# Performance work log

Hardware: AMD Instinct MI355X
Metric: run time of the kernel (lower is better)

Reference implementation:

```python
import jax, jax.numpy as jnp
import numpy as np

N = 100000
E = 1600000
IN_DIM = 128
OUT_DIM = 128
K = 2
LN_EPS = 1e-5


def setup_inputs() -> dict:
    key = jax.random.key(0)
    k1, k2, k3, k4 = jax.random.split(key, 4)
    x = jax.random.normal(k1, (N, IN_DIM), dtype=jnp.float32)
    edge_index = jax.random.randint(k2, (2, E), 0, N, dtype=jnp.int64)
    # LayerNorm params (elementwise affine, torch defaults)
    ln_w = jnp.ones((IN_DIM,), dtype=jnp.float32)
    ln_b = jnp.zeros((IN_DIM,), dtype=jnp.float32)
    # SGConv linear params (torch nn.Linear layout: [out, in])
    bound = 1.0 / np.sqrt(IN_DIM)
    W = jax.random.uniform(k3, (OUT_DIM, IN_DIM), minval=-bound, maxval=bound, dtype=jnp.float32)
    b = jax.random.uniform(k4, (OUT_DIM,), minval=-bound, maxval=bound, dtype=jnp.float32)
    return {"x": x, "edge_index": edge_index, "ln_w": ln_w, "ln_b": ln_b, "W": W, "b": b}


def _layer_norm(x, w, b):
    mu = jnp.mean(x, axis=-1, keepdims=True)
    var = jnp.mean(jnp.square(x - mu), axis=-1, keepdims=True)
    return (x - mu) * jax.lax.rsqrt(var + LN_EPS) * w + b


def _sgc_propagate(x, edge_index):
    # gcn_norm with added self-loops: A_hat = D^{-1/2} (A + I) D^{-1/2}
    src, dst = edge_index[0], edge_index[1]
    loop = jnp.arange(N, dtype=src.dtype)
    src_a = jnp.concatenate([src, loop])
    dst_a = jnp.concatenate([dst, loop])
    deg = jax.ops.segment_sum(jnp.ones((E + N,), dtype=x.dtype), dst_a, num_segments=N)
    dinv = jnp.where(deg > 0, jax.lax.rsqrt(jnp.maximum(deg, 1e-12)), 0.0)
    w = dinv[src_a] * dinv[dst_a]  # [E+N]
    for _ in range(K):
        x = jax.ops.segment_sum(x[src_a] * w[:, None], dst_a, num_segments=N)
    return x


def reference(x, edge_index, ln_w, ln_b, W, b):
    y = _layer_norm(x, ln_w, ln_b)
    y = _sgc_propagate(y, edge_index)
    return y @ W.T + b
```

## Files before the change

kernel.cpp:

```cpp
#include <hip/hip_runtime.h>
#include <hip/hip_fp16.h>

#define DIM 128
#define BKT_SHIFT 8
#define BKT_NODES 256
#define CHUNK 4096
#define MAXBUK 1024
#define ZROW 136

typedef _Float16 half8 __attribute__((ext_vector_type(8)));
typedef float f32x4 __attribute__((ext_vector_type(4)));


__global__ __launch_bounds__(1024) void k_s1_hist(const int* __restrict__ ei, int* __restrict__ H,
                                                  int E, int NBUK, int NBLK) {
    __shared__ int hist[MAXBUK];
    int b = blockIdx.x, tid = threadIdx.x;
    for (int i = tid; i < NBUK; i += 1024) hist[i] = 0;
    __syncthreads();
    int e0 = b * CHUNK, e1 = min(e0 + CHUNK, E);
    for (int e = e0 + tid; e < e1; e += 1024) {
        int dst = ei[E + e];
        atomicAdd(&hist[dst >> BKT_SHIFT], 1);
    }
    __syncthreads();
    for (int k = tid; k < NBUK; k += 1024) H[(size_t)k * NBLK + b] = hist[k];
}


__global__ __launch_bounds__(256) void k_scanA(const int* __restrict__ in, int* __restrict__ tmp,
                                               int* __restrict__ bsum, int n) {
    __shared__ int s[256];
    int tid = threadIdx.x;
    int i = blockIdx.x * 256 + tid;
    int v = (i < n) ? in[i] : 0;
    s[tid] = v;
    __syncthreads();
    for (int off = 1; off < 256; off <<= 1) {
        int t = (tid >= off) ? s[tid - off] : 0;
        __syncthreads();
        s[tid] += t;
        __syncthreads();
    }
    if (i < n) tmp[i] = s[tid];
    if (tid == 255) bsum[blockIdx.x] = s[255];
}

__global__ __launch_bounds__(1024) void k_scanB(int* __restrict__ bsum, int nb) {
    __shared__ int s[1024];
    int tid = threadIdx.x;
    int v = (tid < nb) ? bsum[tid] : 0;
    s[tid] = v;
    __syncthreads();
    for (int off = 1; off < 1024; off <<= 1) {
        int t = (tid >= off) ? s[tid - off] : 0;
        __syncthreads();
        s[tid] += t;
        __syncthreads();
    }
    if (tid < nb) bsum[tid] = s[tid] - v;
}

__global__ __launch_bounds__(256) void k_scanE(int* __restrict__ H, const int* __restrict__ tmp,
                                               const int* __restrict__ bsum, int n) {
    int i = blockIdx.x * 256 + threadIdx.x;
    if (i < n) H[i] = bsum[blockIdx.x] + tmp[i] - H[i];
}


__global__ __launch_bounds__(1024) void k_s3_scatter(const int* __restrict__ ei,
                                                     const int* __restrict__ H,
                                                     int* __restrict__ ssrc,
                                                     unsigned char* __restrict__ sdst, int E,
                                                     int NBUK, int NBLK) {
    __shared__ int off[MAXBUK];
    int b = blockIdx.x, tid = threadIdx.x;
    for (int k = tid; k < NBUK; k += 1024) off[k] = H[(size_t)k * NBLK + b];
    __syncthreads();
    int e0 = b * CHUNK, e1 = min(e0 + CHUNK, E);
    for (int e = e0 + tid; e < e1; e += 1024) {
        int src = ei[e];
        int dst = ei[E + e];
        int p = atomicAdd(&off[dst >> BKT_SHIFT], 1);
        ssrc[p] = src;
        sdst[p] = (unsigned char)(dst & (BKT_NODES - 1));
    }
}


__global__ __launch_bounds__(256) void k_s4_build(const int* __restrict__ H,
                                                  const int* __restrict__ ssrc,
                                                  const unsigned char* __restrict__ sdst,
                                                  int* __restrict__ rp, float* __restrict__ dinv,
                                                  int* __restrict__ col, int N, int E, int NBUK,
                                                  int NBLK) {
    __shared__ int cnt[BKT_NODES];
    __shared__ int pos[BKT_NODES];
    __shared__ int s[BKT_NODES];
    int bkt = blockIdx.x, tid = threadIdx.x;
    int base = H[(size_t)bkt * NBLK];
    int endv = (bkt + 1 < NBUK) ? H[(size_t)(bkt + 1) * NBLK] : E;
    int m = endv - base;
    cnt[tid] = 0;
    __syncthreads();
    for (int i = tid; i < m; i += 256) atomicAdd(&cnt[sdst[base + i]], 1);
    __syncthreads();
    int v = cnt[tid];
    s[tid] = v;
    __syncthreads();
    for (int off = 1; off < 256; off <<= 1) {
        int t = (tid >= off) ? s[tid - off] : 0;
        __syncthreads();
        s[tid] += t;
        __syncthreads();
    }
    int excl = s[tid] - v;
    pos[tid] = excl;
    int node = bkt * BKT_NODES + tid;
    if (node < N) {
        rp[node] = base + excl;
        dinv[node] = rsqrtf((float)(v + 1));
    }
    __syncthreads();
    for (int i = tid; i < m; i += 256) {
        int r = atomicAdd(&pos[sdst[base + i]], 1);
        col[base + r] = ssrc[base + i];
    }
    if (bkt == 0 && tid == 0) rp[N] = E;
}


__global__ __launch_bounds__(256) void k_ln(const float* __restrict__ x,
                                            const float* __restrict__ w,
                                            const float* __restrict__ bb,
                                            const float* __restrict__ dinv,
                                            __half2* __restrict__ u, int N) {
    int row = (blockIdx.x * 256 + threadIdx.x) >> 6;
    int lane = threadIdx.x & 63;
    if (row >= N) return;
    float2 v = *(const float2*)(x + (size_t)row * DIM + lane * 2);
    float s = v.x + v.y;
#pragma unroll
    for (int o = 32; o; o >>= 1) s += __shfl_xor(s, o, 64);
    float mu = s * (1.0f / 128.0f);
    float dx0 = v.x - mu, dx1 = v.y - mu;
    float ss = dx0 * dx0 + dx1 * dx1;
#pragma unroll
    for (int o = 32; o; o >>= 1) ss += __shfl_xor(ss, o, 64);
    float rs = rsqrtf(ss * (1.0f / 128.0f) + 1e-5f);
    float2 wv = *(const float2*)(w + lane * 2);
    float2 bv = *(const float2*)(bb + lane * 2);
    float di = dinv[row];
    float o0 = (dx0 * rs * wv.x + bv.x) * di;
    float o1 = (dx1 * rs * wv.y + bv.y) * di;
    u[(size_t)row * 64 + lane] = __floats2half2_rn(o0, o1);
}


__global__ __launch_bounds__(256) void k_prop(const _Float16* __restrict__ X,
                                              _Float16* __restrict__ Y,
                                              const int* __restrict__ rp,
                                              const int* __restrict__ col,
                                              const float* __restrict__ dinv, int N) {
    int tid = threadIdx.x;
    int node = blockIdx.x * 16 + (tid >> 4);
    int q = tid & 15;
    if (node >= N) return;
    const _Float16* xq = X + q * 8;
    half8 selfv = *(const half8*)(xq + (size_t)node * DIM);
    int e0 = rp[node], e1 = rp[node + 1];
    float acc[8];
#pragma unroll
    for (int f = 0; f < 8; f++) acc[f] = 0.f;
    int e = e0;
    for (; e + 7 < e1; e += 8) {
        int s0 = col[e + 0], s1 = col[e + 1], s2 = col[e + 2], s3 = col[e + 3];
        int s4 = col[e + 4], s5 = col[e + 5], s6 = col[e + 6], s7 = col[e + 7];
        half8 g0 = *(const half8*)(xq + (size_t)s0 * DIM);
        half8 g1 = *(const half8*)(xq + (size_t)s1 * DIM);
        half8 g2 = *(const half8*)(xq + (size_t)s2 * DIM);
        half8 g3 = *(const half8*)(xq + (size_t)s3 * DIM);
        half8 g4 = *(const half8*)(xq + (size_t)s4 * DIM);
        half8 g5 = *(const half8*)(xq + (size_t)s5 * DIM);
        half8 g6 = *(const half8*)(xq + (size_t)s6 * DIM);
        half8 g7 = *(const half8*)(xq + (size_t)s7 * DIM);
#pragma unroll
        for (int f = 0; f < 8; f++)
            acc[f] += (((float)g0[f] + (float)g1[f]) + ((float)g2[f] + (float)g3[f])) +
                      (((float)g4[f] + (float)g5[f]) + ((float)g6[f] + (float)g7[f]));
    }
    for (; e + 1 < e1; e += 2) {
        int s0 = col[e], s1 = col[e + 1];
        half8 g0 = *(const half8*)(xq + (size_t)s0 * DIM);
        half8 g1 = *(const half8*)(xq + (size_t)s1 * DIM);
#pragma unroll
        for (int f = 0; f < 8; f++) acc[f] += (float)g0[f] + (float)g1[f];
    }
    if (e < e1) {
        int s = col[e];
        half8 g = *(const half8*)(xq + (size_t)s * DIM);
#pragma unroll
        for (int f = 0; f < 8; f++) acc[f] += (float)g[f];
    }
    float di = dinv[node];
    float sc = di * di;
    half8 o;
#pragma unroll
    for (int f = 0; f < 8; f++) o[f] = (_Float16)(((float)selfv[f] + acc[f]) * sc);
    *(half8*)(Y + (size_t)node * DIM + q * 8) = o;
}


__global__ __launch_bounds__(256) void k_packW(const float* __restrict__ W,
                                               _Float16* __restrict__ pack) {
    int t = blockIdx.x * 256 + threadIdx.x;
    if (t >= 2048) return;
    int lane = t & 63, ks = (t >> 6) & 3, tile = t >> 8;
    int wrow = tile * 16 + (lane & 15);
    int wcol = ks * 32 + 8 * (lane >> 4);
    float4 w0 = *(const float4*)(W + wrow * DIM + wcol);
    float4 w1 = *(const float4*)(W + wrow * DIM + wcol + 4);
    _Float16* dst = pack + (size_t)t * 8;
    dst[0] = (_Float16)w0.x; dst[1] = (_Float16)w0.y;
    dst[2] = (_Float16)w0.z; dst[3] = (_Float16)w0.w;
    dst[4] = (_Float16)w1.x; dst[5] = (_Float16)w1.y;
    dst[6] = (_Float16)w1.z; dst[7] = (_Float16)w1.w;
}


__global__ __launch_bounds__(256) void k_prop_mm(const _Float16* __restrict__ X,
                                                 const int* __restrict__ rp,
                                                 const int* __restrict__ col,
                                                 const float* __restrict__ dinv,
                                                 const _Float16* __restrict__ pack,
                                                 const float* __restrict__ bias,
                                                 float* __restrict__ out, int N) {
    __shared__ _Float16 Z[64 * ZROW];
    int tid = threadIdx.x;
    int rB = blockIdx.x * 64;
    int g = tid >> 4;
    int q = tid & 15;
    const _Float16* xq = X + q * 8;
#pragma unroll
    for (int k = 0; k < 4; k++) {
        int lrow = g * 4 + k;
        int node = rB + lrow;
        half8 o;
        if (node < N) {
            half8 selfv = *(const half8*)(xq + (size_t)node * DIM);
            int e0 = rp[node], e1 = rp[node + 1];
            float acc[8];
#pragma unroll
            for (int f = 0; f < 8; f++) acc[f] = 0.f;
            int e = e0;
            for (; e + 7 < e1; e += 8) {
                int s0 = col[e + 0], s1 = col[e + 1], s2 = col[e + 2], s3 = col[e + 3];
                int s4 = col[e + 4], s5 = col[e + 5], s6 = col[e + 6], s7 = col[e + 7];
                half8 g0 = *(const half8*)(xq + (size_t)s0 * DIM);
                half8 g1 = *(const half8*)(xq + (size_t)s1 * DIM);
                half8 g2 = *(const half8*)(xq + (size_t)s2 * DIM);
                half8 g3 = *(const half8*)(xq + (size_t)s3 * DIM);
                half8 g4 = *(const half8*)(xq + (size_t)s4 * DIM);
                half8 g5 = *(const half8*)(xq + (size_t)s5 * DIM);
                half8 g6 = *(const half8*)(xq + (size_t)s6 * DIM);
                half8 g7 = *(const half8*)(xq + (size_t)s7 * DIM);
#pragma unroll
                for (int f = 0; f < 8; f++)
                    acc[f] += (((float)g0[f] + (float)g1[f]) + ((float)g2[f] + (float)g3[f])) +
                              (((float)g4[f] + (float)g5[f]) + ((float)g6[f] + (float)g7[f]));
            }
            for (; e + 1 < e1; e += 2) {
                int s0 = col[e], s1 = col[e + 1];
                half8 g0 = *(const half8*)(xq + (size_t)s0 * DIM);
                half8 g1 = *(const half8*)(xq + (size_t)s1 * DIM);
#pragma unroll
                for (int f = 0; f < 8; f++) acc[f] += (float)g0[f] + (float)g1[f];
            }
            if (e < e1) {
                int s = col[e];
                half8 gg = *(const half8*)(xq + (size_t)s * DIM);
#pragma unroll
                for (int f = 0; f < 8; f++) acc[f] += (float)gg[f];
            }
            float sc = dinv[node];
#pragma unroll
            for (int f = 0; f < 8; f++) o[f] = (_Float16)(((float)selfv[f] + acc[f]) * sc);
        } else {
#pragma unroll
            for (int f = 0; f < 8; f++) o[f] = (_Float16)0;
        }
        *(half8*)(&Z[lrow * ZROW + q * 8]) = o;
    }
    __syncthreads();
    int wave = tid >> 6;
    int lane = tid & 63;
    int rw = wave * 16;
    half8 a[4];
#pragma unroll
    for (int ks = 0; ks < 4; ks++)
        a[ks] = *(const half8*)(&Z[(rw + (lane & 15)) * ZROW + ks * 32 + (lane >> 4) * 8]);
    int row0 = rB + rw + (lane >> 4) * 4;
#pragma unroll
    for (int tile = 0; tile < 8; tile++) {
        f32x4 d = {0.f, 0.f, 0.f, 0.f};
#pragma unroll
        for (int ks = 0; ks < 4; ks++) {
            half8 bf = *(const half8*)(pack + ((size_t)((tile * 4 + ks) * 64 + lane)) * 8);
            d = __builtin_amdgcn_mfma_f32_16x16x32_f16(a[ks], bf, d, 0, 0, 0);
        }
        int c = tile * 16 + (lane & 15);
        float bv = bias[c];
#pragma unroll
        for (int j = 0; j < 4; j++) {
            int rr = row0 + j;
            if (rr < N) out[(size_t)rr * DIM + c] = d[j] + bv;
        }
    }
}


extern "C" void kernel_launch(void* const* d_in, const int* in_sizes, int n_in, void* d_out,
                              int out_size, void* d_ws, size_t ws_size, hipStream_t stream) {
    const float* x = (const float*)d_in[0];
    const int* ei = (const int*)d_in[1];
    const float* ln_w = (const float*)d_in[2];
    const float* ln_b = (const float*)d_in[3];
    const float* W = (const float*)d_in[4];
    const float* b = (const float*)d_in[5];
    float* out = (float*)d_out;

    int N = in_sizes[0] / DIM;
    int E = in_sizes[1] / 2;

    int NBUK = (N + BKT_NODES - 1) / BKT_NODES;
    int NBLK = (E + CHUNK - 1) / CHUNK;
    int M = NBUK * NBLK;
    int gScan = (M + 255) / 256;

    char* p = (char*)d_ws;
    auto carve = [&](size_t bytes) {
        void* r = (void*)p;
        p += (bytes + 255) & ~(size_t)255;
        return r;
    };
    __half* u0 = (__half*)carve((size_t)N * DIM * 2);
    __half* u1 = (__half*)carve((size_t)N * DIM * 2);
    _Float16* pack = (_Float16*)carve(DIM * DIM * 2);
    int* H = (int*)carve((size_t)M * 4);
    float* dinv = (float*)carve((size_t)N * 4);
    int* rp = (int*)carve((size_t)(N + 1) * 4);
    int* tmp = (int*)carve((size_t)(N > M ? N : M) * 4);
    int* bsum = (int*)carve(1024 * 4);
    int* col = (int*)carve((size_t)E * 4);

    int* ssrc = (int*)u1;
    unsigned char* sdst = (unsigned char*)u1 + ((size_t)E * 4 + 255 & ~(size_t)255);

    int gW = (N + 3) / 4;
    int gP = (N + 15) / 16;
    int gM = (N + 63) / 64;

    k_s1_hist<<<NBLK, 1024, 0, stream>>>(ei, H, E, NBUK, NBLK);
    k_scanA<<<gScan, 256, 0, stream>>>(H, tmp, bsum, M);
    k_scanB<<<1, 1024, 0, stream>>>(bsum, gScan);
    k_scanE<<<gScan, 256, 0, stream>>>(H, tmp, bsum, M);
    k_s3_scatter<<<NBLK, 1024, 0, stream>>>(ei, H, ssrc, sdst, E, NBUK, NBLK);
    k_s4_build<<<NBUK, 256, 0, stream>>>(H, ssrc, sdst, rp, dinv, col, N, E, NBUK, NBLK);
    k_packW<<<8, 256, 0, stream>>>(W, pack);
    k_ln<<<gW, 256, 0, stream>>>(x, ln_w, ln_b, dinv, (__half2*)u0, N);
    k_prop<<<gP, 256, 0, stream>>>((const _Float16*)u0, (_Float16*)u1, rp, col, dinv, N);
    k_prop_mm<<<gM, 256, 0, stream>>>((const _Float16*)u1, rp, col, dinv, pack, b, out, N);
}
```

Measured before the change: 219.5 us.

## Fold scan finalize into consumers and balance prop_mm rows via shared counter

Removes the k_scanE launch by computing exclusive bucket offsets on the fly (bsum + tmp - H) inside the scatter and build kernels. In k_prop_mm, the fixed assignment of four rows per 16-lane group is replaced by dynamic row claiming through an LDS atomic counter, to even out per-row degree imbalance within a block. This saves one launch and adds an extra global read per offset, plus an LDS atomic and a shuffle per row, and the loop is no longer unrolled.

```diff
diff --git a/kernel.cpp b/kernel.cpp
--- a/kernel.cpp
+++ b/kernel.cpp
@@ -61,21 +61,24 @@
     if (tid < nb) bsum[tid] = s[tid] - v;
 }
 
-__global__ __launch_bounds__(256) void k_scanE(int* __restrict__ H, const int* __restrict__ tmp,
-                                               const int* __restrict__ bsum, int n) {
-    int i = blockIdx.x * 256 + threadIdx.x;
-    if (i < n) H[i] = bsum[blockIdx.x] + tmp[i] - H[i];
+__device__ __forceinline__ int h_excl(const int* H, const int* tmp, const int* bsum, int i) {
+    return bsum[i >> 8] + tmp[i] - H[i];
 }
 
 
 __global__ __launch_bounds__(1024) void k_s3_scatter(const int* __restrict__ ei,
                                                      const int* __restrict__ H,
+                                                     const int* __restrict__ tmp,
+                                                     const int* __restrict__ bsum,
                                                      int* __restrict__ ssrc,
                                                      unsigned char* __restrict__ sdst, int E,
                                                      int NBUK, int NBLK) {
     __shared__ int off[MAXBUK];
     int b = blockIdx.x, tid = threadIdx.x;
-    for (int k = tid; k < NBUK; k += 1024) off[k] = H[(size_t)k * NBLK + b];
+    for (int k = tid; k < NBUK; k += 1024) {
+        int i = k * NBLK + b;
+        off[k] = h_excl(H, tmp, bsum, i);
+    }
     __syncthreads();
     int e0 = b * CHUNK, e1 = min(e0 + CHUNK, E);
     for (int e = e0 + tid; e < e1; e += 1024) {
@@ -89,6 +92,8 @@
 
 
 __global__ __launch_bounds__(256) void k_s4_build(const int* __restrict__ H,
+                                                  const int* __restrict__ tmp,
+                                                  const int* __restrict__ bsum,
                                                   const int* __restrict__ ssrc,
                                                   const unsigned char* __restrict__ sdst,
                                                   int* __restrict__ rp, float* __restrict__ dinv,
@@ -98,8 +103,8 @@
     __shared__ int pos[BKT_NODES];
     __shared__ int s[BKT_NODES];
     int bkt = blockIdx.x, tid = threadIdx.x;
-    int base = H[(size_t)bkt * NBLK];
-    int endv = (bkt + 1 < NBUK) ? H[(size_t)(bkt + 1) * NBLK] : E;
+    int base = h_excl(H, tmp, bsum, bkt * NBLK);
+    int endv = (bkt + 1 < NBUK) ? h_excl(H, tmp, bsum, (bkt + 1) * NBLK) : E;
     int m = endv - base;
     cnt[tid] = 0;
     __syncthreads();
@@ -236,15 +241,19 @@
                                                  const float* __restrict__ bias,
                                                  float* __restrict__ out, int N) {
     __shared__ _Float16 Z[64 * ZROW];
+    __shared__ int ctr;
     int tid = threadIdx.x;
+    if (tid == 0) ctr = 0;
+    __syncthreads();
     int rB = blockIdx.x * 64;
-    int g = tid >> 4;
     int q = tid & 15;
     const _Float16* xq = X + q * 8;
-#pragma unroll
-    for (int k = 0; k < 4; k++) {
-        int lrow = g * 4 + k;
-        int node = rB + lrow;
+    for (;;) {
+        int k = 0;
+        if ((tid & 15) == 0) k = atomicAdd(&ctr, 1);
+        k = __shfl(k, tid & 48, 64);
+        if (k >= 64) break;
+        int node = rB + k;
         half8 o;
         if (node < N) {
             half8 selfv = *(const half8*)(xq + (size_t)node * DIM);
@@ -289,7 +298,7 @@
 #pragma unroll
             for (int f = 0; f < 8; f++) o[f] = (_Float16)0;
         }
-        *(half8*)(&Z[lrow * ZROW + q * 8]) = o;
+        *(half8*)(&Z[k * ZROW + q * 8]) = o;
     }
     __syncthreads();
     int wave = tid >> 6;
@@ -363,9 +372,9 @@
     k_s1_hist<<<NBLK, 1024, 0, stream>>>(ei, H, E, NBUK, NBLK);
     k_scanA<<<gScan, 256, 0, stream>>>(H, tmp, bsum, M);
     k_scanB<<<1, 1024, 0, stream>>>(bsum, gScan);
-    k_scanE<<<gScan, 256, 0, stream>>>(H, tmp, bsum, M);
-    k_s3_scatter<<<NBLK, 1024, 0, stream>>>(ei, H, ssrc, sdst, E, NBUK, NBLK);
-    k_s4_build<<<NBUK, 256, 0, stream>>>(H, ssrc, sdst, rp, dinv, col, N, E, NBUK, NBLK);
+    k_s3_scatter<<<NBLK, 1024, 0, stream>>>(ei, H, tmp, bsum, ssrc, sdst, E, NBUK, NBLK);
+    k_s4_build<<<NBUK, 256, 0, stream>>>(H, tmp, bsum, ssrc, sdst, rp, dinv, col, N, E, NBUK,
+                                         NBLK);
     k_packW<<<8, 256, 0, stream>>>(W, pack);
     k_ln<<<gW, 256, 0, stream>>>(x, ln_w, ln_b, dinv, (__half2*)u0, N);
     k_prop<<<gP, 256, 0, stream>>>((const _Float16*)u0, (_Float16*)u1, rp, col, dinv, N);
```

Result: no change. 222.3 us (+1.3%).
